# Performance work log

Hardware: AMD Instinct MI355X
Metric: run time of the kernel (lower is better)

Reference implementation:

```python
import jax, jax.numpy as jnp
import numpy as np

B, T, C, H = 4, 2048, 768, 12
HD = C // H  # 64
EPS = 1e-5


def layer_norm(x, g, b):
    mu = jnp.mean(x, axis=-1, keepdims=True)
    var = jnp.var(x, axis=-1, keepdims=True)
    return (x - mu) * jax.lax.rsqrt(var + EPS) * g + b


def setup_inputs() -> dict:
    key = jax.random.key(0)
    ks = jax.random.split(key, 14)
    s_c = 1.0 / np.sqrt(C)
    s_4c = 1.0 / np.sqrt(4 * C)
    return {
        "x": jax.random.normal(ks[0], (B, T, C), jnp.float32),
        # per-head Q/K/V projections stacked over heads [H, C, HD]
        "wq": jax.random.uniform(ks[1], (H, C, HD), jnp.float32, -s_c, s_c),
        "bq": jnp.zeros((H, HD), jnp.float32),
        "wk": jax.random.uniform(ks[2], (H, C, HD), jnp.float32, -s_c, s_c),
        "bk": jnp.zeros((H, HD), jnp.float32),
        "wv": jax.random.uniform(ks[3], (H, C, HD), jnp.float32, -s_c, s_c),
        "bv": jnp.zeros((H, HD), jnp.float32),
        "w_proj": jax.random.uniform(ks[4], (C, C), jnp.float32, -s_c, s_c),
        "b_proj": jnp.zeros((C,), jnp.float32),
        "w1": jax.random.uniform(ks[5], (C, 4 * C), jnp.float32, -s_c, s_c),
        "b1": jnp.zeros((4 * C,), jnp.float32),
        "w2": jax.random.uniform(ks[6], (4 * C, C), jnp.float32, -s_4c, s_4c),
        "b2": jnp.zeros((C,), jnp.float32),
        "g1": jnp.ones((C,), jnp.float32),
        "beta1": jnp.zeros((C,), jnp.float32),
        "g2": jnp.ones((C,), jnp.float32),
        "beta2": jnp.zeros((C,), jnp.float32),
    }


def reference(x, wq, bq, wk, bk, wv, bv, w_proj, b_proj, w1, b1, w2, b2, g1, beta1, g2, beta2):
    # --- attention sublayer ---
    h = layer_norm(x, g1, beta1)
    q = jnp.einsum('btc,hcd->bhtd', h, wq) + bq[None, :, None, :]
    k = jnp.einsum('btc,hcd->bhtd', h, wk) + bk[None, :, None, :]
    v = jnp.einsum('btc,hcd->bhtd', h, wv) + bv[None, :, None, :]
    # NOTE: source applies NO 1/sqrt(head_size) scaling
    scores = jnp.einsum('bhtd,bhsd->bhts', q, k)  # [B,H,T,T]
    causal = jnp.tril(jnp.ones((T, T), bool))
    scores = jnp.where(causal, scores, -jnp.inf)
    wei = jax.nn.softmax(scores, axis=-1)
    attn = jnp.einsum('bhts,bhsd->bhtd', wei, v)  # [B,H,T,HD]
    attn = attn.transpose(0, 2, 1, 3).reshape(B, T, C)  # concat heads
    x = x + attn @ w_proj + b_proj
    # --- MLP sublayer ---
    h2 = layer_norm(x, g2, beta2)
    x = x + jax.nn.relu(h2 @ w1 + b1) @ w2 + b2
    return x
```

## Files before the change

### kernel.cpp

```cpp
#include <hip/hip_runtime.h>
#include <hip/hip_bf16.h>
#include <math.h>

#define BB 4
#define TT 2048
#define CC 768
#define HH 12
#define HDIM 64
#define C4 3072
#define MM (BB*TT)
#define EPSL 1e-5f

typedef __bf16 bf16x8 __attribute__((ext_vector_type(8)));
typedef __bf16 bf16x4 __attribute__((ext_vector_type(4)));
typedef float f32x4 __attribute__((ext_vector_type(4)));

__device__ __forceinline__ ushort f2bf(float f) {
    union { float f; unsigned u; } v; v.f = f;
    unsigned r = v.u + 0x7fffu + ((v.u >> 16) & 1u);
    return (ushort)(r >> 16);
}

__device__ __forceinline__ void glds16(const void* g, void* l) {
    __builtin_amdgcn_global_load_lds(
        (const __attribute__((address_space(1))) void*)g,
        (__attribute__((address_space(3))) void*)l, 16, 0, 0);
}

#define WVM(N) asm volatile("s_waitcnt vmcnt(" #N ")" ::: "memory")
#define WLG0   asm volatile("s_waitcnt lgkmcnt(0)" ::: "memory")

__device__ __forceinline__ void pbar() {
    __builtin_amdgcn_sched_barrier(0);
    __builtin_amdgcn_s_barrier();
    __builtin_amdgcn_sched_barrier(0);
}

__global__ __launch_bounds__(256) void ln_k(const float* __restrict__ X,
                                            const float* __restrict__ G,
                                            const float* __restrict__ Be,
                                            ushort* __restrict__ O)
{
    int row = blockIdx.x;
    const float* xr = X + (size_t)row * CC;
    int t = threadIdx.x;
    float v0 = xr[t], v1 = xr[t + 256], v2 = xr[t + 512];
    float s  = v0 + v1 + v2;
    float sq = v0*v0 + v1*v1 + v2*v2;
    #pragma unroll
    for (int off = 32; off; off >>= 1) {
        s  += __shfl_xor(s,  off);
        sq += __shfl_xor(sq, off);
    }
    __shared__ float red[8];
    int wv = t >> 6, ln = t & 63;
    if (ln == 0) { red[wv] = s; red[4 + wv] = sq; }
    __syncthreads();
    s  = red[0] + red[1] + red[2] + red[3];
    sq = red[4] + red[5] + red[6] + red[7];
    float mu  = s * (1.0f / CC);
    float var = sq * (1.0f / CC) - mu * mu;
    float rs  = rsqrtf(var + EPSL);
    ushort* orow = O + (size_t)row * CC;
    orow[t]       = f2bf((v0 - mu) * rs * G[t]       + Be[t]);
    orow[t + 256] = f2bf((v1 - mu) * rs * G[t + 256] + Be[t + 256]);
    orow[t + 512] = f2bf((v2 - mu) * rs * G[t + 512] + Be[t + 512]);
}

__global__ __launch_bounds__(256) void ln_add_k(float* __restrict__ X,
                                                const float* __restrict__ P,
                                                const float* __restrict__ G,
                                                const float* __restrict__ Be,
                                                ushort* __restrict__ O)
{
    int row = blockIdx.x;
    float* xr = X + (size_t)row * CC;
    const float* pr = P + (size_t)row * CC;
    int t = threadIdx.x;
    float v0 = xr[t]       + pr[t];
    float v1 = xr[t + 256] + pr[t + 256];
    float v2 = xr[t + 512] + pr[t + 512];
    xr[t] = v0; xr[t + 256] = v1; xr[t + 512] = v2;
    float s  = v0 + v1 + v2;
    float sq = v0*v0 + v1*v1 + v2*v2;
    #pragma unroll
    for (int off = 32; off; off >>= 1) {
        s  += __shfl_xor(s,  off);
        sq += __shfl_xor(sq, off);
    }
    __shared__ float red[8];
    int wv = t >> 6, ln = t & 63;
    if (ln == 0) { red[wv] = s; red[4 + wv] = sq; }
    __syncthreads();
    s  = red[0] + red[1] + red[2] + red[3];
    sq = red[4] + red[5] + red[6] + red[7];
    float mu  = s * (1.0f / CC);
    float var = sq * (1.0f / CC) - mu * mu;
    float rs  = rsqrtf(var + EPSL);
    ushort* orow = O + (size_t)row * CC;
    orow[t]       = f2bf((v0 - mu) * rs * G[t]       + Be[t]);
    orow[t + 256] = f2bf((v1 - mu) * rs * G[t + 256] + Be[t + 256]);
    orow[t + 512] = f2bf((v2 - mu) * rs * G[t + 512] + Be[t + 512]);
}

__global__ __launch_bounds__(256) void addto_k(float* __restrict__ o,
                                               const float* __restrict__ p,
                                               int n4)
{
    int i = blockIdx.x * 256 + threadIdx.x;
    int stride = gridDim.x * 256;
    for (; i < n4; i += stride) {
        float4 a = ((const float4*)o)[i];
        float4 b = ((const float4*)p)[i];
        a.x += b.x; a.y += b.y; a.z += b.z; a.w += b.w;
        ((float4*)o)[i] = a;
    }
}

template<int MODE>
__global__ __launch_bounds__(256) void repack_k(const float* __restrict__ W,
                                                ushort* __restrict__ WT,
                                                int K, int N, int outStride)
{
    __shared__ float tl[64][65];
    int n0 = blockIdx.x * 64, k0 = blockIdx.y * 64;
    int c = threadIdx.x & 63, rr = threadIdx.x >> 6;
    #pragma unroll
    for (int i = 0; i < 16; ++i) {
        int r = i * 4 + rr;
        float v;
        if (MODE == 0) v = W[(size_t)(k0 + r) * N + n0 + c];
        else           v = W[((size_t)(n0 >> 6) * CC + k0 + r) * 64 + c];
        tl[r][c] = v;
    }
    __syncthreads();
    #pragma unroll
    for (int i = 0; i < 16; ++i) {
        int r = i * 4 + rr;
        WT[(size_t)(n0 + r) * outStride + k0 + c] = f2bf(tl[c][r]);
    }
}

template<int EPI>
__global__ __launch_bounds__(512, 2) void gemm8p(
    const ushort* __restrict__ A, const ushort* __restrict__ BT,
    int M, int N, int K,
    void* __restrict__ ov0, void* __restrict__ ov1, void* __restrict__ ov2,
    const float* __restrict__ bias0, const float* __restrict__ bias1,
    const float* __restrict__ bias2,
    const float* __restrict__ resid, ushort* __restrict__ obf,
    float* __restrict__ part)
{
    __shared__ ushort lds[2][2][256 * 64];

    int nbx = gridDim.x;
    int nwg = nbx * gridDim.y * gridDim.z;
    int orig = (blockIdx.z * gridDim.y + blockIdx.y) * nbx + blockIdx.x;
    int cpx = nwg >> 3;
    int swz = (orig & 7) * cpx + (orig >> 3);
    int zi = swz / (nbx * gridDim.y);
    int rem = swz - zi * nbx * gridDim.y;
    int bn = rem % nbx, bm = rem / nbx;

    int tid = threadIdx.x;
    int lane = tid & 63;
    int w = tid >> 6;
    int wrow = (w >> 2) * 128, wcol = (w & 3) * 64;
    int fr = lane & 15, kh = lane >> 4;
    int rxor = (fr & 7) * 8;

    const size_t aR0 = (size_t)bm * 256;
    const size_t bR0 = (size_t)bn * 256;
    const int Ksl = K / (int)gridDim.z;
    const int koff = zi * Ksl;
    const int nt = Ksl >> 6;

    int srow = tid >> 3;
    int scol = (tid & 7) * 8;
    int gcol = koff + (scol ^ ((srow & 7) * 8));

    f32x4 acc[8][4] = {};

    {
        glds16(BT + (bR0 +   0 + srow) * K + gcol, &lds[0][1][(  0 + srow) * 64 + scol]);
        glds16(BT + (bR0 +  64 + srow) * K + gcol, &lds[0][1][( 64 + srow) * 64 + scol]);
        glds16(BT + (bR0 + 128 + srow) * K + gcol, &lds[0][1][(128 + srow) * 64 + scol]);
        glds16(BT + (bR0 + 192 + srow) * K + gcol, &lds[0][1][(192 + srow) * 64 + scol]);
        glds16(A  + (aR0 +   0 + srow) * K + gcol, &lds[0][0][(  0 + srow) * 64 + scol]);
        glds16(A  + (aR0 + 128 + srow) * K + gcol, &lds[0][0][(128 + srow) * 64 + scol]);
        glds16(A  + (aR0 +  64 + srow) * K + gcol, &lds[0][0][( 64 + srow) * 64 + scol]);
        glds16(A  + (aR0 + 192 + srow) * K + gcol, &lds[0][0][(192 + srow) * 64 + scol]);
    }
    WVM(2);
    pbar();

    for (int t = 0; t < nt; ++t) {
        int slot = t & 1, nslot = slot ^ 1;
        int kst = gcol + ((t + 1) << 6);
        bool st = (t + 1) < nt;
        const ushort* Asl = &lds[slot][0][0];
        const ushort* Bsl = &lds[slot][1][0];
        bf16x8 aF[4][2];
        #pragma unroll
        for (int p = 0; p < 4; ++p) {
            const int rh = p >> 1, ch = p & 1;
            if (ch == 0) {
                #pragma unroll
                for (int i = 0; i < 4; ++i)
                    #pragma unroll
                    for (int k2 = 0; k2 < 2; ++k2) {
                        int R = wrow + rh * 64 + i * 16 + fr;
                        aF[i][k2] = *(const bf16x8*)&Asl[R * 64 + ((k2 * 32 + kh * 8) ^ rxor)];
                    }
            }
            bf16x8 bF[2][2];
            #pragma unroll
            for (int j2 = 0; j2 < 2; ++j2)
                #pragma unroll
                for (int k2 = 0; k2 < 2; ++k2) {
                    int Rb = wcol + ch * 32 + j2 * 16 + fr;
                    bF[j2][k2] = *(const bf16x8*)&Bsl[Rb * 64 + ((k2 * 32 + kh * 8) ^ rxor)];
                }
            if (st) {
                if (p == 0) {
                    glds16(BT + (bR0 +   0 + srow) * K + kst, &lds[nslot][1][(  0 + srow) * 64 + scol]);
                    glds16(BT + (bR0 +  64 + srow) * K + kst, &lds[nslot][1][( 64 + srow) * 64 + scol]);
                    glds16(BT + (bR0 + 128 + srow) * K + kst, &lds[nslot][1][(128 + srow) * 64 + scol]);
                    glds16(BT + (bR0 + 192 + srow) * K + kst, &lds[nslot][1][(192 + srow) * 64 + scol]);
                } else if (p == 1) {
                    glds16(A  + (aR0 +   0 + srow) * K + kst, &lds[nslot][0][(  0 + srow) * 64 + scol]);
                    glds16(A  + (aR0 + 128 + srow) * K + kst, &lds[nslot][0][(128 + srow) * 64 + scol]);
                    glds16(A  + (aR0 +  64 + srow) * K + kst, &lds[nslot][0][( 64 + srow) * 64 + scol]);
                    glds16(A  + (aR0 + 192 + srow) * K + kst, &lds[nslot][0][(192 + srow) * 64 + scol]);
                }
            }
            __builtin_amdgcn_s_setprio(1);
            #pragma unroll
            for (int i = 0; i < 4; ++i)
                #pragma unroll
                for (int j2 = 0; j2 < 2; ++j2)
                    #pragma unroll
                    for (int k2 = 0; k2 < 2; ++k2)
                        acc[rh * 4 + i][ch * 2 + j2] = __builtin_amdgcn_mfma_f32_16x16x32_bf16(
                            aF[i][k2], bF[j2][k2], acc[rh * 4 + i][ch * 2 + j2], 0, 0, 0);
            __builtin_amdgcn_s_setprio(0);
            if (p == 1) { if (st) { WVM(8); } else { WVM(0); } }
            else if (p == 3) { if (st) { WVM(2); } }
            WLG0;
            pbar();
        }
    }

    if (gridDim.z > 1 && zi > 0) {
        #pragma unroll
        for (int ri = 0; ri < 8; ++ri) {
            int row0 = bm * 256 + wrow + ri * 16 + kh * 4;
            #pragma unroll
            for (int cj = 0; cj < 4; ++cj) {
                int col = bn * 256 + wcol + cj * 16 + fr;
                #pragma unroll
                for (int r = 0; r < 4; ++r)
                    part[(size_t)(row0 + r) * N + col] = acc[ri][cj][r];
            }
        }
    } else if (EPI == 1) {
        int seg = bn / 3;
        ushort* op = (ushort*)(seg == 0 ? ov0 : (seg == 1 ? ov1 : ov2));
        const float* bsp = seg == 0 ? bias0 : (seg == 1 ? bias1 : bias2);
        int cb = (bn - seg * 3) * 256 + wcol;
        int h = cb >> 6;
        #pragma unroll
        for (int ri = 0; ri < 8; ++ri) {
            int row0 = bm * 256 + wrow + ri * 16 + kh * 4;
            int b = row0 >> 11;
            int t0 = row0 & (TT - 1);
            #pragma unroll
            for (int cj = 0; cj < 4; ++cj) {
                int d = cj * 16 + fr;
                float bsv = bsp[h * 64 + d];
                #pragma unroll
                for (int r = 0; r < 4; ++r)
                    op[((size_t)(b * HH + h) * TT + t0 + r) * 64 + d] =
                        f2bf(acc[ri][cj][r] + bsv);
            }
        }
    } else if (EPI == 2) {
        float* o0 = (float*)ov0;
        #pragma unroll
        for (int ri = 0; ri < 8; ++ri) {
            int row0 = bm * 256 + wrow + ri * 16 + kh * 4;
            #pragma unroll
            for (int cj = 0; cj < 4; ++cj) {
                int col = bn * 256 + wcol + cj * 16 + fr;
                float bsv = bias0[col];
                #pragma unroll
                for (int r = 0; r < 4; ++r) {
                    size_t idx = (size_t)(row0 + r) * N + col;
                    o0[idx] = acc[ri][cj][r] + bsv + resid[idx];
                }
            }
        }
    } else {
        #pragma unroll
        for (int ri = 0; ri < 8; ++ri) {
            int row0 = bm * 256 + wrow + ri * 16 + kh * 4;
            #pragma unroll
            for (int cj = 0; cj < 4; ++cj) {
                int col = bn * 256 + wcol + cj * 16 + fr;
                float bsv = bias0[col];
                #pragma unroll
                for (int r = 0; r < 4; ++r) {
                    float v = fmaxf(acc[ri][cj][r] + bsv, 0.f);
                    obf[(size_t)(row0 + r) * N + col] = f2bf(v);
                }
            }
        }
    }
}

__global__ __launch_bounds__(256) void vtrans_k(const ushort* __restrict__ V,
                                                ushort* __restrict__ Vt)
{
    __shared__ ushort tl[64][72];
    int blk = blockIdx.x;
    int tt = blk & 31, bh = blk >> 5;
    size_t base = (size_t)bh * TT * 64;
    int t0 = tt * 64;
    int e = threadIdx.x;
    int rr = e >> 3, cc8 = (e & 7) * 8;
    #pragma unroll
    for (int p = 0; p < 2; ++p) {
        int t = p * 32 + rr;
        *(uint4*)&tl[t][cc8] = *(const uint4*)&V[base + (size_t)(t0 + t) * 64 + cc8];
    }
    __syncthreads();
    #pragma unroll
    for (int p = 0; p < 2; ++p) {
        int d = p * 32 + rr;
        ushort tmp[8];
        #pragma unroll
        for (int i = 0; i < 8; ++i) tmp[i] = tl[cc8 + i][d];
        *(uint4*)&Vt[base + (size_t)d * TT + t0 + cc8] = *(uint4*)tmp;
    }
}

__global__ __launch_bounds__(256) void attn_k(const ushort* __restrict__ Q,
                                              const ushort* __restrict__ Kb,
                                              const ushort* __restrict__ Vt,
                                              ushort* __restrict__ Ob)
{
    __shared__ ushort Kl[64][64];
    __shared__ ushort Vl[64][64];
    __shared__ ushort Pl[4][16][68];

    int orig = blockIdx.x;
    int swz = (orig & 7) * 96 + (orig >> 3);
    int pair = swz & 15;
    int bh = swz >> 4;
    int b = bh / HH, h = bh - b * HH;
    int tid = threadIdx.x, lane = tid & 63, w = tid >> 6;
    int c = lane & 15, g = lane >> 4;
    size_t base = (size_t)bh * TT * 64;
    int srow = tid >> 3;
    int scol = (tid & 7) * 8;
    int sw0 = scol ^ ((srow & 7) * 8);
    int sw1 = scol ^ (((srow + 32) & 7) * 8);
    int rxk = (c & 7) * 8;
    const float LOG2E = 1.44269504088896340736f;

    #pragma unroll
    for (int sel = 0; sel < 2; ++sel) {
        int qt = sel ? (31 - pair) : pair;
        int q0 = qt * 64;

        bf16x8 aq[2];
        #pragma unroll
        for (int kc = 0; kc < 2; ++kc) {
            bf16x8 raw = *(const bf16x8*)&Q[base + (size_t)(q0 + w * 16 + c) * 64 + kc * 32 + g * 8];
            #pragma unroll
            for (int e = 0; e < 8; ++e)
                raw[e] = (__bf16)((float)raw[e] * LOG2E);
            aq[kc] = raw;
        }

        f32x4 oa[4] = {};
        float mrun[4] = {-INFINITY, -INFINITY, -INFINITY, -INFINITY};
        float lrun[4] = {0.f, 0.f, 0.f, 0.f};

        uint4 k0r = *(const uint4*)&Kb[base + (size_t)srow * 64 + scol];
        uint4 k1r = *(const uint4*)&Kb[base + (size_t)(32 + srow) * 64 + scol];
        uint4 v0r = *(const uint4*)&Vt[base + (size_t)srow * TT + scol];
        uint4 v1r = *(const uint4*)&Vt[base + (size_t)(32 + srow) * TT + scol];

        for (int kv0 = 0; kv0 <= q0; kv0 += 64) {
            __syncthreads();
            *(uint4*)&Kl[srow][sw0]      = k0r;
            *(uint4*)&Kl[32 + srow][sw1] = k1r;
            *(uint4*)&Vl[srow][sw0]      = v0r;
            *(uint4*)&Vl[32 + srow][sw1] = v1r;
            __syncthreads();
            if (kv0 + 64 <= q0) {
                int kn = kv0 + 64;
                k0r = *(const uint4*)&Kb[base + (size_t)(kn + srow) * 64 + scol];
                k1r = *(const uint4*)&Kb[base + (size_t)(kn + 32 + srow) * 64 + scol];
                v0r = *(const uint4*)&Vt[base + (size_t)srow * TT + kn + scol];
                v1r = *(const uint4*)&Vt[base + (size_t)(32 + srow) * TT + kn + scol];
            }

            f32x4 sa[4] = {};
            #pragma unroll
            for (int kc = 0; kc < 2; ++kc)
                #pragma unroll
                for (int j = 0; j < 4; ++j) {
                    bf16x8 kf = *(const bf16x8*)&Kl[j * 16 + c][(kc * 32 + g * 8) ^ rxk];
                    sa[j] = __builtin_amdgcn_mfma_f32_16x16x32_bf16(aq[kc], kf, sa[j], 0, 0, 0);
                }

            if (kv0 == q0) {
                #pragma unroll
                for (int j = 0; j < 4; ++j)
                    #pragma unroll
                    for (int r = 0; r < 4; ++r)
                        if (j * 16 + c > w * 16 + g * 4 + r) sa[j][r] = -1e30f;
            }

            float vlmax = sa[0][0];
            #pragma unroll
            for (int j = 0; j < 4; ++j)
                #pragma unroll
                for (int r = 0; r < 4; ++r) vlmax = fmaxf(vlmax, sa[j][r]);
            float mmin = fminf(fminf(mrun[0], mrun[1]), fminf(mrun[2], mrun[3]));
            if (!__all(vlmax <= mmin + 11.5f)) {
                #pragma unroll
                for (int r = 0; r < 4; ++r) {
                    float m0 = fmaxf(fmaxf(sa[0][r], sa[1][r]), fmaxf(sa[2][r], sa[3][r]));
                    #pragma unroll
                    for (int off = 8; off; off >>= 1) m0 = fmaxf(m0, __shfl_xor(m0, off));
                    float mnew = fmaxf(mrun[r], m0);
                    float sc = __builtin_amdgcn_exp2f(mrun[r] - mnew);
                    lrun[r] *= sc;
                    #pragma unroll
                    for (int j = 0; j < 4; ++j) oa[j][r] *= sc;
                    mrun[r] = mnew;
                }
            }
            #pragma unroll
            for (int r = 0; r < 4; ++r) {
                float ps = 0.f;
                #pragma unroll
                for (int j = 0; j < 4; ++j) {
                    float p = __builtin_amdgcn_exp2f(sa[j][r] - mrun[r]);
                    sa[j][r] = p;
                    ps += p;
                }
                lrun[r] += ps;
            }

            #pragma unroll
            for (int r = 0; r < 4; ++r)
                #pragma unroll
                for (int j = 0; j < 4; ++j)
                    Pl[w][g * 4 + r][j * 16 + c] = (ushort)__builtin_bit_cast(unsigned short, (__bf16)sa[j][r]);

            bf16x8 pf[2];
            #pragma unroll
            for (int kc = 0; kc < 2; ++kc) {
                bf16x4 lo = *(const bf16x4*)&Pl[w][c][kc * 32 + g * 8];
                bf16x4 hi = *(const bf16x4*)&Pl[w][c][kc * 32 + g * 8 + 4];
                pf[kc] = __builtin_shufflevector(lo, hi, 0, 1, 2, 3, 4, 5, 6, 7);
            }

            #pragma unroll
            for (int kc = 0; kc < 2; ++kc)
                #pragma unroll
                for (int j = 0; j < 4; ++j) {
                    bf16x8 vf = *(const bf16x8*)&Vl[j * 16 + c][(kc * 32 + g * 8) ^ rxk];
                    oa[j] = __builtin_amdgcn_mfma_f32_16x16x32_bf16(pf[kc], vf, oa[j], 0, 0, 0);
                }
        }

        float inv[4];
        #pragma unroll
        for (int r = 0; r < 4; ++r) {
            float l = lrun[r];
            #pragma unroll
            for (int off = 8; off; off >>= 1) l += __shfl_xor(l, off);
            inv[r] = 1.0f / l;
        }
        size_t orow = (size_t)b * TT + q0 + w * 16;
        #pragma unroll
        for (int j = 0; j < 4; ++j)
            #pragma unroll
            for (int r = 0; r < 4; ++r) {
                float v = oa[j][r] * inv[r];
                Ob[(orow + g * 4 + r) * CC + h * 64 + j * 16 + c] = f2bf(v);
            }
    }
}

extern "C" void kernel_launch(void* const* d_in, const int* in_sizes, int n_in,
                              void* d_out, int out_size, void* d_ws, size_t ws_size,
                              hipStream_t stream)
{
    const float* x   = (const float*)d_in[0];
    const float* wq  = (const float*)d_in[1];
    const float* bq  = (const float*)d_in[2];
    const float* wk  = (const float*)d_in[3];
    const float* bk  = (const float*)d_in[4];
    const float* wvw = (const float*)d_in[5];
    const float* bv  = (const float*)d_in[6];
    const float* wp  = (const float*)d_in[7];
    const float* bp  = (const float*)d_in[8];
    const float* w1  = (const float*)d_in[9];
    const float* b1  = (const float*)d_in[10];
    const float* w2  = (const float*)d_in[11];
    const float* b2  = (const float*)d_in[12];
    const float* g1  = (const float*)d_in[13];
    const float* be1 = (const float*)d_in[14];
    const float* g2  = (const float*)d_in[15];
    const float* be2 = (const float*)d_in[16];

    float* out = (float*)d_out;
    const size_t S = (size_t)MM * CC;

    ushort* wsu   = (ushort*)d_ws;
    ushort* WTqkv = wsu;
    ushort* WTp   = WTqkv + (size_t)2304 * 768;
    ushort* WT1   = WTp   + (size_t)768 * 768;
    ushort* WT2   = WT1   + (size_t)3072 * 768;
    ushort* hbf   = WT2   + (size_t)768 * 3072;
    ushort* attnb = hbf   + S;
    ushort* qb    = attnb + S;
    ushort* kb    = qb + S;
    ushort* vb    = kb + S;
    ushort* vtb   = vb + S;
    ushort* midb  = qb;
    float*  part_proj = (float*)qb;
    float*  part_w2   = (float*)hbf;

    dim3 rg(12, 12);
    repack_k<1><<<rg, 256, 0, stream>>>(wq,  WTqkv,                      768, 768, 768);
    repack_k<1><<<rg, 256, 0, stream>>>(wk,  WTqkv + (size_t)768*768,    768, 768, 768);
    repack_k<1><<<rg, 256, 0, stream>>>(wvw, WTqkv + (size_t)2*768*768,  768, 768, 768);
    repack_k<0><<<rg, 256, 0, stream>>>(wp,  WTp, 768, 768, 768);
    repack_k<0><<<dim3(48, 12), 256, 0, stream>>>(w1, WT1, 768, 3072, 768);
    repack_k<0><<<dim3(12, 48), 256, 0, stream>>>(w2, WT2, 3072, 768, 3072);

    ln_k<<<MM, 256, 0, stream>>>(x, g1, be1, hbf);
    gemm8p<1><<<dim3(9, 32, 1), 512, 0, stream>>>(hbf, WTqkv, MM, 2304, CC,
        qb, kb, vb, bq, bk, bv, nullptr, nullptr, nullptr);
    vtrans_k<<<48 * 32, 256, 0, stream>>>(vb, vtb);
    attn_k<<<48 * 16, 256, 0, stream>>>(qb, kb, vtb, attnb);
    gemm8p<2><<<dim3(3, 32, 2), 512, 0, stream>>>(attnb, WTp, MM, CC, CC,
        out, nullptr, nullptr, bp, nullptr, nullptr, x, nullptr, part_proj);

    ln_add_k<<<MM, 256, 0, stream>>>(out, part_proj, g2, be2, hbf);
    gemm8p<3><<<dim3(12, 32, 1), 512, 0, stream>>>(hbf, WT1, MM, C4, CC,
        nullptr, nullptr, nullptr, b1, nullptr, nullptr, nullptr, midb, nullptr);
    gemm8p<2><<<dim3(3, 32, 2), 512, 0, stream>>>(midb, WT2, MM, CC, C4,
        out, nullptr, nullptr, b2, nullptr, nullptr, out, nullptr, part_w2);
    addto_k<<<2048, 256, 0, stream>>>(out, part_w2, MM * CC / 4);
}
```

Before: 299.7 us.

## Restructure GEMM to 128x256 tiles with 3-stage K=32 LDS pipeline

The shared bf16 GEMM kernel drops from 256x256 tiles with a K=64 double buffer to 128x256 tiles with K=32 steps and a triple-buffered LDS ring. The LDS swizzle changes to match. Launch bounds are raised to 3 workgroups per CU and the grids double along M. The goal is more resident workgroups, lower register and LDS use, and deeper prefetch to hide global-load latency. The cost is less reuse of the B tile, twice as many barriers per unit of K work, and smaller MFMA batches between syncs.

```diff
diff --git a/kernel.cpp b/kernel.cpp
--- a/kernel.cpp
+++ b/kernel.cpp
@@ -142,7 +142,7 @@
 }
 
 template<int EPI>
-__global__ __launch_bounds__(512, 2) void gemm8p(
+__global__ __launch_bounds__(512, 3) void gemm3s(
     const ushort* __restrict__ A, const ushort* __restrict__ BT,
     int M, int N, int K,
     void* __restrict__ ov0, void* __restrict__ ov1, void* __restrict__ ov2,
@@ -151,7 +151,7 @@
     const float* __restrict__ resid, ushort* __restrict__ obf,
     float* __restrict__ part)
 {
-    __shared__ ushort lds[2][2][256 * 64];
+    __shared__ ushort lds[3 * 12288];
 
     int nbx = gridDim.x;
     int nwg = nbx * gridDim.y * gridDim.z;
@@ -165,102 +165,73 @@
     int tid = threadIdx.x;
     int lane = tid & 63;
     int w = tid >> 6;
-    int wrow = (w >> 2) * 128, wcol = (w & 3) * 64;
+    int wrow = (w >> 2) * 64, wcol = (w & 3) * 64;
     int fr = lane & 15, kh = lane >> 4;
-    int rxor = (fr & 7) * 8;
-
-    const size_t aR0 = (size_t)bm * 256;
+    int rxor = ((fr >> 1) & 3) * 8;
+
+    const size_t aR0 = (size_t)bm * 128;
     const size_t bR0 = (size_t)bn * 256;
     const int Ksl = K / (int)gridDim.z;
     const int koff = zi * Ksl;
-    const int nt = Ksl >> 6;
-
-    int srow = tid >> 3;
-    int scol = (tid & 7) * 8;
-    int gcol = koff + (scol ^ ((srow & 7) * 8));
-
-    f32x4 acc[8][4] = {};
-
-    {
-        glds16(BT + (bR0 +   0 + srow) * K + gcol, &lds[0][1][(  0 + srow) * 64 + scol]);
-        glds16(BT + (bR0 +  64 + srow) * K + gcol, &lds[0][1][( 64 + srow) * 64 + scol]);
-        glds16(BT + (bR0 + 128 + srow) * K + gcol, &lds[0][1][(128 + srow) * 64 + scol]);
-        glds16(BT + (bR0 + 192 + srow) * K + gcol, &lds[0][1][(192 + srow) * 64 + scol]);
-        glds16(A  + (aR0 +   0 + srow) * K + gcol, &lds[0][0][(  0 + srow) * 64 + scol]);
-        glds16(A  + (aR0 + 128 + srow) * K + gcol, &lds[0][0][(128 + srow) * 64 + scol]);
-        glds16(A  + (aR0 +  64 + srow) * K + gcol, &lds[0][0][( 64 + srow) * 64 + scol]);
-        glds16(A  + (aR0 + 192 + srow) * K + gcol, &lds[0][0][(192 + srow) * 64 + scol]);
-    }
-    WVM(2);
+    const int nt = Ksl >> 5;
+
+    int srow = tid >> 2;
+    int scol = (tid & 3) * 8;
+    int sxor = scol ^ (((tid >> 3) & 3) * 8);
+
+    f32x4 acc[4][4] = {};
+
+    auto stage = [&](int slot, int t) {
+        int kb = koff + (t << 5) + sxor;
+        ushort* As = lds + slot * 12288;
+        glds16(A  + (aR0 + srow) * K + kb,       As + srow * 32 + scol);
+        glds16(BT + (bR0 + srow) * K + kb,       As + 4096 + srow * 32 + scol);
+        glds16(BT + (bR0 + 128 + srow) * K + kb, As + 4096 + (128 + srow) * 32 + scol);
+    };
+
+    stage(0, 0);
+    stage(1, 1);
+    WVM(3);
     pbar();
 
+    int slot = 0;
     for (int t = 0; t < nt; ++t) {
-        int slot = t & 1, nslot = slot ^ 1;
-        int kst = gcol + ((t + 1) << 6);
-        bool st = (t + 1) < nt;
-        const ushort* Asl = &lds[slot][0][0];
-        const ushort* Bsl = &lds[slot][1][0];
-        bf16x8 aF[4][2];
-        #pragma unroll
-        for (int p = 0; p < 4; ++p) {
-            const int rh = p >> 1, ch = p & 1;
-            if (ch == 0) {
-                #pragma unroll
-                for (int i = 0; i < 4; ++i)
-                    #pragma unroll
-                    for (int k2 = 0; k2 < 2; ++k2) {
-                        int R = wrow + rh * 64 + i * 16 + fr;
-                        aF[i][k2] = *(const bf16x8*)&Asl[R * 64 + ((k2 * 32 + kh * 8) ^ rxor)];
-                    }
-            }
-            bf16x8 bF[2][2];
-            #pragma unroll
-            for (int j2 = 0; j2 < 2; ++j2)
-                #pragma unroll
-                for (int k2 = 0; k2 < 2; ++k2) {
-                    int Rb = wcol + ch * 32 + j2 * 16 + fr;
-                    bF[j2][k2] = *(const bf16x8*)&Bsl[Rb * 64 + ((k2 * 32 + kh * 8) ^ rxor)];
-                }
-            if (st) {
-                if (p == 0) {
-                    glds16(BT + (bR0 +   0 + srow) * K + kst, &lds[nslot][1][(  0 + srow) * 64 + scol]);
-                    glds16(BT + (bR0 +  64 + srow) * K + kst, &lds[nslot][1][( 64 + srow) * 64 + scol]);
-                    glds16(BT + (bR0 + 128 + srow) * K + kst, &lds[nslot][1][(128 + srow) * 64 + scol]);
-                    glds16(BT + (bR0 + 192 + srow) * K + kst, &lds[nslot][1][(192 + srow) * 64 + scol]);
-                } else if (p == 1) {
-                    glds16(A  + (aR0 +   0 + srow) * K + kst, &lds[nslot][0][(  0 + srow) * 64 + scol]);
-                    glds16(A  + (aR0 + 128 + srow) * K + kst, &lds[nslot][0][(128 + srow) * 64 + scol]);
-                    glds16(A  + (aR0 +  64 + srow) * K + kst, &lds[nslot][0][( 64 + srow) * 64 + scol]);
-                    glds16(A  + (aR0 + 192 + srow) * K + kst, &lds[nslot][0][(192 + srow) * 64 + scol]);
-                }
-            }
-            __builtin_amdgcn_s_setprio(1);
-            #pragma unroll
-            for (int i = 0; i < 4; ++i)
-                #pragma unroll
-                for (int j2 = 0; j2 < 2; ++j2)
-                    #pragma unroll
-                    for (int k2 = 0; k2 < 2; ++k2)
-                        acc[rh * 4 + i][ch * 2 + j2] = __builtin_amdgcn_mfma_f32_16x16x32_bf16(
-                            aF[i][k2], bF[j2][k2], acc[rh * 4 + i][ch * 2 + j2], 0, 0, 0);
-            __builtin_amdgcn_s_setprio(0);
-            if (p == 1) { if (st) { WVM(8); } else { WVM(0); } }
-            else if (p == 3) { if (st) { WVM(2); } }
-            WLG0;
-            pbar();
-        }
+        const ushort* As = lds + slot * 12288;
+        const ushort* Bs = As + 4096;
+        bf16x8 aF[4], bF[4];
+        #pragma unroll
+        for (int i = 0; i < 4; ++i)
+            aF[i] = *(const bf16x8*)&As[(wrow + i * 16 + fr) * 32 + ((kh * 8) ^ rxor)];
+        #pragma unroll
+        for (int j = 0; j < 4; ++j)
+            bF[j] = *(const bf16x8*)&Bs[(wcol + j * 16 + fr) * 32 + ((kh * 8) ^ rxor)];
+        if (t + 2 < nt) {
+            int ns = slot + 2; if (ns >= 3) ns -= 3;
+            stage(ns, t + 2);
+        }
+        __builtin_amdgcn_s_setprio(1);
+        #pragma unroll
+        for (int i = 0; i < 4; ++i)
+            #pragma unroll
+            for (int j = 0; j < 4; ++j)
+                acc[i][j] = __builtin_amdgcn_mfma_f32_16x16x32_bf16(aF[i], bF[j], acc[i][j], 0, 0, 0);
+        __builtin_amdgcn_s_setprio(0);
+        if (t + 2 < nt) { WVM(3); } else { WVM(0); }
+        WLG0;
+        pbar();
+        slot = slot + 1 == 3 ? 0 : slot + 1;
     }
 
     if (gridDim.z > 1 && zi > 0) {
         #pragma unroll
-        for (int ri = 0; ri < 8; ++ri) {
-            int row0 = bm * 256 + wrow + ri * 16 + kh * 4;
-            #pragma unroll
-            for (int cj = 0; cj < 4; ++cj) {
-                int col = bn * 256 + wcol + cj * 16 + fr;
+        for (int i = 0; i < 4; ++i) {
+            int row0 = bm * 128 + wrow + i * 16 + kh * 4;
+            #pragma unroll
+            for (int j = 0; j < 4; ++j) {
+                int col = bn * 256 + wcol + j * 16 + fr;
                 #pragma unroll
                 for (int r = 0; r < 4; ++r)
-                    part[(size_t)(row0 + r) * N + col] = acc[ri][cj][r];
+                    part[(size_t)(row0 + r) * N + col] = acc[i][j][r];
             }
         }
     } else if (EPI == 1) {
@@ -270,47 +241,47 @@
         int cb = (bn - seg * 3) * 256 + wcol;
         int h = cb >> 6;
         #pragma unroll
-        for (int ri = 0; ri < 8; ++ri) {
-            int row0 = bm * 256 + wrow + ri * 16 + kh * 4;
+        for (int i = 0; i < 4; ++i) {
+            int row0 = bm * 128 + wrow + i * 16 + kh * 4;
             int b = row0 >> 11;
             int t0 = row0 & (TT - 1);
             #pragma unroll
-            for (int cj = 0; cj < 4; ++cj) {
-                int d = cj * 16 + fr;
+            for (int j = 0; j < 4; ++j) {
+                int d = j * 16 + fr;
                 float bsv = bsp[h * 64 + d];
                 #pragma unroll
                 for (int r = 0; r < 4; ++r)
                     op[((size_t)(b * HH + h) * TT + t0 + r) * 64 + d] =
-                        f2bf(acc[ri][cj][r] + bsv);
+                        f2bf(acc[i][j][r] + bsv);
             }
         }
     } else if (EPI == 2) {
         float* o0 = (float*)ov0;
         #pragma unroll
-        for (int ri = 0; ri < 8; ++ri) {
-            int row0 = bm * 256 + wrow + ri * 16 + kh * 4;
-            #pragma unroll
-            for (int cj = 0; cj < 4; ++cj) {
-                int col = bn * 256 + wcol + cj * 16 + fr;
+        for (int i = 0; i < 4; ++i) {
+            int row0 = bm * 128 + wrow + i * 16 + kh * 4;
+            #pragma unroll
+            for (int j = 0; j < 4; ++j) {
+                int col = bn * 256 + wcol + j * 16 + fr;
                 float bsv = bias0[col];
                 #pragma unroll
                 for (int r = 0; r < 4; ++r) {
                     size_t idx = (size_t)(row0 + r) * N + col;
-                    o0[idx] = acc[ri][cj][r] + bsv + resid[idx];
+                    o0[idx] = acc[i][j][r] + bsv + resid[idx];
                 }
             }
         }
     } else {
         #pragma unroll
-        for (int ri = 0; ri < 8; ++ri) {
-            int row0 = bm * 256 + wrow + ri * 16 + kh * 4;
-            #pragma unroll
-            for (int cj = 0; cj < 4; ++cj) {
-                int col = bn * 256 + wcol + cj * 16 + fr;
+        for (int i = 0; i < 4; ++i) {
+            int row0 = bm * 128 + wrow + i * 16 + kh * 4;
+            #pragma unroll
+            for (int j = 0; j < 4; ++j) {
+                int col = bn * 256 + wcol + j * 16 + fr;
                 float bsv = bias0[col];
                 #pragma unroll
                 for (int r = 0; r < 4; ++r) {
-                    float v = fmaxf(acc[ri][cj][r] + bsv, 0.f);
+                    float v = fmaxf(acc[i][j][r] + bsv, 0.f);
                     obf[(size_t)(row0 + r) * N + col] = f2bf(v);
                 }
             }
@@ -547,17 +518,17 @@
     repack_k<0><<<dim3(12, 48), 256, 0, stream>>>(w2, WT2, 3072, 768, 3072);
 
     ln_k<<<MM, 256, 0, stream>>>(x, g1, be1, hbf);
-    gemm8p<1><<<dim3(9, 32, 1), 512, 0, stream>>>(hbf, WTqkv, MM, 2304, CC,
+    gemm3s<1><<<dim3(9, 64, 1), 512, 0, stream>>>(hbf, WTqkv, MM, 2304, CC,
         qb, kb, vb, bq, bk, bv, nullptr, nullptr, nullptr);
     vtrans_k<<<48 * 32, 256, 0, stream>>>(vb, vtb);
     attn_k<<<48 * 16, 256, 0, stream>>>(qb, kb, vtb, attnb);
-    gemm8p<2><<<dim3(3, 32, 2), 512, 0, stream>>>(attnb, WTp, MM, CC, CC,
+    gemm3s<2><<<dim3(3, 64, 2), 512, 0, stream>>>(attnb, WTp, MM, CC, CC,
         out, nullptr, nullptr, bp, nullptr, nullptr, x, nullptr, part_proj);
 
     ln_add_k<<<MM, 256, 0, stream>>>(out, part_proj, g2, be2, hbf);
-    gemm8p<3><<<dim3(12, 32, 1), 512, 0, stream>>>(hbf, WT1, MM, C4, CC,
+    gemm3s<3><<<dim3(12, 64, 1), 512, 0, stream>>>(hbf, WT1, MM, C4, CC,
         nullptr, nullptr, nullptr, b1, nullptr, nullptr, nullptr, midb, nullptr);
-    gemm8p<2><<<dim3(3, 32, 2), 512, 0, stream>>>(midb, WT2, MM, CC, C4,
+    gemm3s<2><<<dim3(3, 64, 2), 512, 0, stream>>>(midb, WT2, MM, CC, C4,
         out, nullptr, nullptr, b2, nullptr, nullptr, out, nullptr, part_w2);
     addto_k<<<2048, 256, 0, stream>>>(out, part_w2, MM * CC / 4);
 }
```

Result: faster. 289.2 us (-3.5%).
